# Kernel tuning notes

Measured on AMD Instinct MI355X. Metric: run time of the kernel, lower is better.

The kernel has to match this reference:

```python
import jax, jax.numpy as jnp
import numpy as np

S, B, H, K = 2048, 64, 8, 12          # seq_len, input_bits, num_heads, bits per RAM neuron
N_POS = 11                             # bits for relative distance in [0, max_seq_len-1]


def setup_inputs() -> dict:
    key = jax.random.key(0)
    k1, k2, k3, k4, k5 = jax.random.split(key, 5)
    tokens = jax.random.randint(k1, (S, B), 0, 2, dtype=jnp.int32)            # bit tokens
    conn_heads = jax.random.randint(k2, (H, K), 0, 2 * B + N_POS, dtype=jnp.int32)
    head_table = jnp.round(jax.random.uniform(k3, (H, 1 << K))).astype(jnp.float32)  # {0,1} RAM cells
    conn_v = jax.random.randint(k4, (B, K), 0, B, dtype=jnp.int32)
    table_v = jnp.round(jax.random.uniform(k5, (B, 1 << K))).astype(jnp.float32)     # {0,1} RAM cells
    return {"tokens": tokens, "conn_heads": conn_heads, "head_table": head_table,
            "conn_v": conn_v, "table_v": table_v}


def reference(tokens, conn_heads, head_table, conn_v, table_v):
    pow2 = (1 << (K - 1 - jnp.arange(K))).astype(jnp.int32)                 # [K] MSB-first
    tok = tokens.astype(jnp.int32)                                           # [S,B]

    # split each head's 12 connections into query / key / relative-position groups
    grp_q = (conn_heads < B).astype(jnp.int32)
    grp_k = ((conn_heads >= B) & (conn_heads < 2 * B)).astype(jnp.int32)
    grp_p = (conn_heads >= 2 * B).astype(jnp.int32)
    cq = jnp.clip(conn_heads, 0, B - 1)
    ck = jnp.clip(conn_heads - B, 0, B - 1)
    cp = jnp.clip(conn_heads - 2 * B, 0, N_POS - 1)

    # additive address decomposition: addr(i,j,h) = addr_q(i,h)+addr_k(j,h)+addr_p(i-j,h)
    addr_q = (tok[:, cq] * (grp_q * pow2)[None]).sum(-1)                     # [S,H]
    addr_k = (tok[:, ck] * (grp_k * pow2)[None]).sum(-1)                     # [S,H]
    ar = jnp.arange(S)
    posb = ((ar[:, None] >> (N_POS - 1 - jnp.arange(N_POS))[None, :]) & 1).astype(jnp.int32)  # [S,N_POS]
    addr_p = (posb[:, cp] * (grp_p * pow2)[None]).sum(-1)                    # [S,H] indexed by rel dist

    rel = jnp.clip(ar[:, None] - ar[None, :], 0)                             # [S,S]
    addr = addr_q[:, None, :] + addr_k[None, :, :] + addr_p[rel]             # [S,S,H]

    # per-head table lookup, sum over heads = vote counts
    votes = head_table[jnp.arange(H)[None, None, :], addr].sum(-1)           # [S,S]
    causal = ar[None, :] <= ar[:, None]
    votes = jnp.where(causal, votes, 0.0)

    # bit-level value projection: one RAM neuron per output bit
    addr_v = (tok[:, conn_v] * pow2[None, None, :]).sum(-1)                  # [S,B]
    values = table_v[jnp.arange(B)[None, :], addr_v]                         # [S,B]

    # TOP_1 aggregation: first key with max vote; zeros if max vote is 0
    max_vote = votes.max(axis=1)                                             # [S]
    best = jnp.argmax(votes, axis=1)                                         # first occurrence, like the loop
    out = jnp.where((max_vote > 0)[:, None], values[best], 0.0)              # [S,B]
    return out
```

## Files before the change

kernel.cpp:

```cpp
#include <hip/hip_runtime.h>


#define SS 2048
#define BB 64
#define HH 8
#define KK 12
#define NPOS 11
#define TBL 4096
#define TBLW (TBL / 32)

__global__ __launch_bounds__(256) void precompute_kernel(
    const int* __restrict__ tokens,
    const int* __restrict__ conn_heads,
    const float* __restrict__ head_table,
    int* __restrict__ A, int* __restrict__ AK, int* __restrict__ P,
    unsigned int* __restrict__ bits)
{
    int gid = blockIdx.x * blockDim.x + threadIdx.x;
    if (gid < SS * HH) {
        int s = gid >> 3;
        int h = gid & 7;
        int aq = 0, ak = 0, ap = 0;
        #pragma unroll
        for (int k = 0; k < KK; ++k) {
            int c = conn_heads[h * KK + k];
            int sh = KK - 1 - k;
            if (c < BB) {
                aq |= (tokens[s * BB + c] & 1) << sh;
            } else if (c < 2 * BB) {
                ak |= (tokens[s * BB + (c - BB)] & 1) << sh;
            } else {
                int cp = c - 2 * BB;
                ap |= ((s >> (NPOS - 1 - cp)) & 1) << sh;
            }
        }
        A[gid] = aq;
        AK[gid] = ak;
        P[gid] = ap;
    } else {
        int w = gid - SS * HH;
        if (w < HH * TBLW) {
            int h = w >> 7;
            int wi = w & (TBLW - 1);
            unsigned int bv = 0;
            #pragma unroll
            for (int b = 0; b < 32; ++b) {
                if (head_table[h * TBL + wi * 32 + b] > 0.5f) bv |= (1u << b);
            }
            bits[w] = bv;
        }
    }
}

__device__ __forceinline__ int votes8(const unsigned int* sbits,
                                      const int4& q0, const int4& q1,
                                      const int4& k0, const int4& k1,
                                      const int4& p0, const int4& p1)
{
    int v = 0, a;
    a = q0.x | k0.x | p0.x; v += (sbits[0 * TBLW + (a >> 5)] >> (a & 31)) & 1;
    a = q0.y | k0.y | p0.y; v += (sbits[1 * TBLW + (a >> 5)] >> (a & 31)) & 1;
    a = q0.z | k0.z | p0.z; v += (sbits[2 * TBLW + (a >> 5)] >> (a & 31)) & 1;
    a = q0.w | k0.w | p0.w; v += (sbits[3 * TBLW + (a >> 5)] >> (a & 31)) & 1;
    a = q1.x | k1.x | p1.x; v += (sbits[4 * TBLW + (a >> 5)] >> (a & 31)) & 1;
    a = q1.y | k1.y | p1.y; v += (sbits[5 * TBLW + (a >> 5)] >> (a & 31)) & 1;
    a = q1.z | k1.z | p1.z; v += (sbits[6 * TBLW + (a >> 5)] >> (a & 31)) & 1;
    a = q1.w | k1.w | p1.w; v += (sbits[7 * TBLW + (a >> 5)] >> (a & 31)) & 1;
    return v;
}

__global__ __launch_bounds__(256) void vote_kernel(
    const int* __restrict__ A, const int* __restrict__ AK, const int* __restrict__ P,
    const unsigned int* __restrict__ bits_g,
    const int* __restrict__ tokens,
    const int* __restrict__ conn_v,
    const float* __restrict__ table_v,
    float* __restrict__ out)
{
    __shared__ unsigned int sbits[HH * TBLW];
    __shared__ unsigned int skey[2][4];

    const int tid = threadIdx.x;
    const int b = blockIdx.x;
    const int i0 = b;
    const int i1 = SS - 1 - b;

    ((uint4*)sbits)[tid] = ((const uint4*)bits_g)[tid];
    __syncthreads();

    const int4 q00 = *(const int4*)(A + i0 * HH);
    const int4 q01 = *(const int4*)(A + i0 * HH + 4);
    const int4 q10 = *(const int4*)(A + i1 * HH);
    const int4 q11 = *(const int4*)(A + i1 * HH + 4);

    unsigned int key0 = 0u, key1 = 0u;

    for (int j = tid; j <= i0; j += 256) {
        const int4 k0 = *(const int4*)(AK + j * HH);
        const int4 k1 = *(const int4*)(AK + j * HH + 4);
        const int d = i0 - j;
        const int4 p0 = *(const int4*)(P + d * HH);
        const int4 p1 = *(const int4*)(P + d * HH + 4);
        int v = votes8(sbits, q00, q01, k0, k1, p0, p1);
        unsigned int key = ((unsigned)v << 12) | (unsigned)(4095 - j);
        key0 = key0 > key ? key0 : key;
    }
    for (int j = tid; j <= i1; j += 256) {
        const int4 k0 = *(const int4*)(AK + j * HH);
        const int4 k1 = *(const int4*)(AK + j * HH + 4);
        const int d = i1 - j;
        const int4 p0 = *(const int4*)(P + d * HH);
        const int4 p1 = *(const int4*)(P + d * HH + 4);
        int v = votes8(sbits, q10, q11, k0, k1, p0, p1);
        unsigned int key = ((unsigned)v << 12) | (unsigned)(4095 - j);
        key1 = key1 > key ? key1 : key;
    }

    #pragma unroll
    for (int off = 32; off > 0; off >>= 1) {
        unsigned int o0 = (unsigned int)__shfl_xor((int)key0, off, 64);
        unsigned int o1 = (unsigned int)__shfl_xor((int)key1, off, 64);
        key0 = key0 > o0 ? key0 : o0;
        key1 = key1 > o1 ? key1 : o1;
    }
    if ((tid & 63) == 0) {
        skey[0][tid >> 6] = key0;
        skey[1][tid >> 6] = key1;
    }
    __syncthreads();

    if (tid < 128) {
        const int r = tid >> 6;
        const int lane = tid & 63;
        unsigned int ka = skey[r][0] > skey[r][1] ? skey[r][0] : skey[r][1];
        unsigned int kb = skey[r][2] > skey[r][3] ? skey[r][2] : skey[r][3];
        unsigned int kf = ka > kb ? ka : kb;
        const int row = r ? i1 : i0;
        float o = 0.0f;
        if ((kf >> 12) > 0) {
            const int best = 4095 - (int)(kf & 4095u);
            int av = 0;
            #pragma unroll
            for (int k = 0; k < KK; ++k) {
                int c = conn_v[lane * KK + k];
                av |= (tokens[best * BB + c] & 1) << (KK - 1 - k);
            }
            o = table_v[lane * TBL + av];
        }
        out[row * BB + lane] = o;
    }
}

extern "C" void kernel_launch(void* const* d_in, const int* in_sizes, int n_in,
                              void* d_out, int out_size, void* d_ws, size_t ws_size,
                              hipStream_t stream) {
    const int*   tokens     = (const int*)d_in[0];
    const int*   conn_heads = (const int*)d_in[1];
    const float* head_table = (const float*)d_in[2];
    const int*   conn_v     = (const int*)d_in[3];
    const float* table_v    = (const float*)d_in[4];
    float* out = (float*)d_out;

    int* ws = (int*)d_ws;
    int* A  = ws;
    int* AK = ws + SS * HH;
    int* P  = ws + 2 * SS * HH;
    unsigned int* bits = (unsigned int*)(ws + 3 * SS * HH);

    const int total1 = SS * HH + HH * TBLW;
    precompute_kernel<<<(total1 + 255) / 256, 256, 0, stream>>>(
        tokens, conn_heads, head_table, A, AK, P, bits);
    vote_kernel<<<SS / 2, 256, 0, stream>>>(
        A, AK, P, bits, tokens, conn_v, table_v, out);
}
```

Baseline: 73.58 us.

## Pack addresses as u16 and exit vote scan early on max vote

Stores the per-position query, key and position address parts as 16-bit values, so each row's eight heads load as one uint4 instead of two int4. The vote loop now walks chunks of 256 keys in ascending order. When any thread sees the maximum vote of 8, a shared flag stops further chunks, since the first key reaching the maximum always wins the argmax. This is meant to skip most of the causal scan for long rows. In exchange it adds two block barriers per chunk and depends on data where a full vote actually occurs.

```diff
diff --git a/kernel.cpp b/kernel.cpp
--- a/kernel.cpp
+++ b/kernel.cpp
@@ -9,12 +9,16 @@
 #define TBL 4096
 #define TBLW (TBL / 32)
 
+typedef unsigned short u16;
+typedef unsigned int u32;
+
+
 __global__ __launch_bounds__(256) void precompute_kernel(
     const int* __restrict__ tokens,
     const int* __restrict__ conn_heads,
     const float* __restrict__ head_table,
-    int* __restrict__ A, int* __restrict__ AK, int* __restrict__ P,
-    unsigned int* __restrict__ bits)
+    u16* __restrict__ A16, u16* __restrict__ AK16, u16* __restrict__ P16,
+    u32* __restrict__ bits)
 {
     int gid = blockIdx.x * blockDim.x + threadIdx.x;
     if (gid < SS * HH) {
@@ -34,15 +38,15 @@
                 ap |= ((s >> (NPOS - 1 - cp)) & 1) << sh;
             }
         }
-        A[gid] = aq;
-        AK[gid] = ak;
-        P[gid] = ap;
+        A16[gid]  = (u16)aq;
+        AK16[gid] = (u16)ak;
+        P16[gid]  = (u16)ap;
     } else {
         int w = gid - SS * HH;
         if (w < HH * TBLW) {
             int h = w >> 7;
             int wi = w & (TBLW - 1);
-            unsigned int bv = 0;
+            u32 bv = 0;
             #pragma unroll
             for (int b = 0; b < 32; ++b) {
                 if (head_table[h * TBL + wi * 32 + b] > 0.5f) bv |= (1u << b);
@@ -52,33 +56,41 @@
     }
 }
 
-__device__ __forceinline__ int votes8(const unsigned int* sbits,
-                                      const int4& q0, const int4& q1,
-                                      const int4& k0, const int4& k1,
-                                      const int4& p0, const int4& p1)
+__device__ __forceinline__ int votes_packed(const u32* sbits,
+                                            const uint4& q, const uint4& kk, const uint4& pp)
 {
-    int v = 0, a;
-    a = q0.x | k0.x | p0.x; v += (sbits[0 * TBLW + (a >> 5)] >> (a & 31)) & 1;
-    a = q0.y | k0.y | p0.y; v += (sbits[1 * TBLW + (a >> 5)] >> (a & 31)) & 1;
-    a = q0.z | k0.z | p0.z; v += (sbits[2 * TBLW + (a >> 5)] >> (a & 31)) & 1;
-    a = q0.w | k0.w | p0.w; v += (sbits[3 * TBLW + (a >> 5)] >> (a & 31)) & 1;
-    a = q1.x | k1.x | p1.x; v += (sbits[4 * TBLW + (a >> 5)] >> (a & 31)) & 1;
-    a = q1.y | k1.y | p1.y; v += (sbits[5 * TBLW + (a >> 5)] >> (a & 31)) & 1;
-    a = q1.z | k1.z | p1.z; v += (sbits[6 * TBLW + (a >> 5)] >> (a & 31)) & 1;
-    a = q1.w | k1.w | p1.w; v += (sbits[7 * TBLW + (a >> 5)] >> (a & 31)) & 1;
+    int v = 0;
+    u32 w, a0, a1;
+    w = q.x | kk.x | pp.x;
+    a0 = w & 0xFFFFu; a1 = w >> 16;
+    v += (sbits[0 * TBLW + (a0 >> 5)] >> (a0 & 31)) & 1;
+    v += (sbits[1 * TBLW + (a1 >> 5)] >> (a1 & 31)) & 1;
+    w = q.y | kk.y | pp.y;
+    a0 = w & 0xFFFFu; a1 = w >> 16;
+    v += (sbits[2 * TBLW + (a0 >> 5)] >> (a0 & 31)) & 1;
+    v += (sbits[3 * TBLW + (a1 >> 5)] >> (a1 & 31)) & 1;
+    w = q.z | kk.z | pp.z;
+    a0 = w & 0xFFFFu; a1 = w >> 16;
+    v += (sbits[4 * TBLW + (a0 >> 5)] >> (a0 & 31)) & 1;
+    v += (sbits[5 * TBLW + (a1 >> 5)] >> (a1 & 31)) & 1;
+    w = q.w | kk.w | pp.w;
+    a0 = w & 0xFFFFu; a1 = w >> 16;
+    v += (sbits[6 * TBLW + (a0 >> 5)] >> (a0 & 31)) & 1;
+    v += (sbits[7 * TBLW + (a1 >> 5)] >> (a1 & 31)) & 1;
     return v;
 }
 
 __global__ __launch_bounds__(256) void vote_kernel(
-    const int* __restrict__ A, const int* __restrict__ AK, const int* __restrict__ P,
-    const unsigned int* __restrict__ bits_g,
+    const u16* __restrict__ A16, const u16* __restrict__ AK16, const u16* __restrict__ P16,
+    const u32* __restrict__ bits_g,
     const int* __restrict__ tokens,
     const int* __restrict__ conn_v,
     const float* __restrict__ table_v,
     float* __restrict__ out)
 {
-    __shared__ unsigned int sbits[HH * TBLW];
-    __shared__ unsigned int skey[2][4];
+    __shared__ u32 sbits[HH * TBLW];
+    __shared__ u32 skey[2][4];
+    __shared__ int sdone[2];
 
     const int tid = threadIdx.x;
     const int b = blockIdx.x;
@@ -86,40 +98,50 @@
     const int i1 = SS - 1 - b;
 
     ((uint4*)sbits)[tid] = ((const uint4*)bits_g)[tid];
+    if (tid == 0) { sdone[0] = 0; sdone[1] = 0; }
     __syncthreads();
 
-    const int4 q00 = *(const int4*)(A + i0 * HH);
-    const int4 q01 = *(const int4*)(A + i0 * HH + 4);
-    const int4 q10 = *(const int4*)(A + i1 * HH);
-    const int4 q11 = *(const int4*)(A + i1 * HH + 4);
+    const uint4 q0 = *(const uint4*)(A16 + i0 * HH);
+    const uint4 q1 = *(const uint4*)(A16 + i1 * HH);
 
-    unsigned int key0 = 0u, key1 = 0u;
+    u32 key0 = 0u, key1 = 0u;
+    int done0 = 0, done1 = 0;
+    const int nc0 = (i0 >> 8) + 1;
+    const int nc1 = (i1 >> 8) + 1;
 
-    for (int j = tid; j <= i0; j += 256) {
-        const int4 k0 = *(const int4*)(AK + j * HH);
-        const int4 k1 = *(const int4*)(AK + j * HH + 4);
-        const int d = i0 - j;
-        const int4 p0 = *(const int4*)(P + d * HH);
-        const int4 p1 = *(const int4*)(P + d * HH + 4);
-        int v = votes8(sbits, q00, q01, k0, k1, p0, p1);
-        unsigned int key = ((unsigned)v << 12) | (unsigned)(4095 - j);
-        key0 = key0 > key ? key0 : key;
-    }
-    for (int j = tid; j <= i1; j += 256) {
-        const int4 k0 = *(const int4*)(AK + j * HH);
-        const int4 k1 = *(const int4*)(AK + j * HH + 4);
-        const int d = i1 - j;
-        const int4 p0 = *(const int4*)(P + d * HH);
-        const int4 p1 = *(const int4*)(P + d * HH + 4);
-        int v = votes8(sbits, q10, q11, k0, k1, p0, p1);
-        unsigned int key = ((unsigned)v << 12) | (unsigned)(4095 - j);
-        key1 = key1 > key ? key1 : key;
+    for (int c = 0; ; ++c) {
+        const int j = (c << 8) + tid;
+        int f0 = 0, f1 = 0;
+        if (!done0 && j <= i0) {
+            const uint4 kk = *(const uint4*)(AK16 + j * HH);
+            const uint4 pp = *(const uint4*)(P16 + (i0 - j) * HH);
+            int v = votes_packed(sbits, q0, kk, pp);
+            u32 key = ((u32)v << 12) | (u32)(4095 - j);
+            key0 = key0 > key ? key0 : key;
+            f0 = (v == HH);
+        }
+        if (!done1 && j <= i1) {
+            const uint4 kk = *(const uint4*)(AK16 + j * HH);
+            const uint4 pp = *(const uint4*)(P16 + (i1 - j) * HH);
+            int v = votes_packed(sbits, q1, kk, pp);
+            u32 key = ((u32)v << 12) | (u32)(4095 - j);
+            key1 = key1 > key ? key1 : key;
+            f1 = (v == HH);
+        }
+        if (f0) sdone[0] = 1;
+        if (f1) sdone[1] = 1;
+        __syncthreads();
+        const int d0 = sdone[0], d1 = sdone[1];
+        __syncthreads();
+        done0 = d0 | ((c + 1) >= nc0);
+        done1 = d1 | ((c + 1) >= nc1);
+        if (done0 && done1) break;
     }
 
     #pragma unroll
     for (int off = 32; off > 0; off >>= 1) {
-        unsigned int o0 = (unsigned int)__shfl_xor((int)key0, off, 64);
-        unsigned int o1 = (unsigned int)__shfl_xor((int)key1, off, 64);
+        u32 o0 = (u32)__shfl_xor((int)key0, off, 64);
+        u32 o1 = (u32)__shfl_xor((int)key1, off, 64);
         key0 = key0 > o0 ? key0 : o0;
         key1 = key1 > o1 ? key1 : o1;
     }
@@ -132,9 +154,9 @@
     if (tid < 128) {
         const int r = tid >> 6;
         const int lane = tid & 63;
-        unsigned int ka = skey[r][0] > skey[r][1] ? skey[r][0] : skey[r][1];
-        unsigned int kb = skey[r][2] > skey[r][3] ? skey[r][2] : skey[r][3];
-        unsigned int kf = ka > kb ? ka : kb;
+        u32 ka = skey[r][0] > skey[r][1] ? skey[r][0] : skey[r][1];
+        u32 kb = skey[r][2] > skey[r][3] ? skey[r][2] : skey[r][3];
+        u32 kf = ka > kb ? ka : kb;
         const int row = r ? i1 : i0;
         float o = 0.0f;
         if ((kf >> 12) > 0) {
@@ -162,14 +184,14 @@
     float* out = (float*)d_out;
 
     int* ws = (int*)d_ws;
-    int* A  = ws;
-    int* AK = ws + SS * HH;
-    int* P  = ws + 2 * SS * HH;
-    unsigned int* bits = (unsigned int*)(ws + 3 * SS * HH);
+    u16* A16  = (u16*)ws;
+    u16* AK16 = (u16*)(ws + 1 * SS * HH / 2);
+    u16* P16  = (u16*)(ws + 2 * SS * HH / 2);
+    u32* bits = (u32*)(ws + 3 * SS * HH / 2);
 
     const int total1 = SS * HH + HH * TBLW;
     precompute_kernel<<<(total1 + 255) / 256, 256, 0, stream>>>(
-        tokens, conn_heads, head_table, A, AK, P, bits);
+        tokens, conn_heads, head_table, A16, AK16, P16, bits);
     vote_kernel<<<SS / 2, 256, 0, stream>>>(
-        A, AK, P, bits, tokens, conn_v, table_v, out);
+        A16, AK16, P16, bits, tokens, conn_v, table_v, out);
 }
```

Result: no change. 72.69 us (-1.2%).
